# Performance work log

Measured on AMD Instinct MI355X. Metric: run time of the kernel, lower is better.

## Reference

```python
import jax, jax.numpy as jnp
import numpy as np

N, E, B = 50000, 400000, 128
F_IN, EDIM, EMB, H = 64, 8, 64, 4
HC = EMB * H  # 256
L = 3          # gnn_layers
DN = 256       # dense_neurons
NEG_SLOPE = 0.2
EPS = 1e-5


def setup_inputs():
    key = jax.random.key(0)
    ks = jax.random.split(key, 32)
    s = 0.05
    d = {}
    d["x"] = jax.random.normal(ks[0], (N, F_IN), jnp.float32)
    d["edge_index"] = jax.random.randint(ks[1], (2, E), 0, N, jnp.int32)
    d["edge_attr"] = jax.random.normal(ks[2], (E, EDIM), jnp.float32)
    d["mol_formal_charge"] = jax.random.normal(ks[3], (B,), jnp.float32)
    d["mol_nrot"] = jax.random.normal(ks[4], (B,), jnp.float32)
    d["batch_index"] = jnp.sort(jax.random.randint(ks[5], (N,), 0, B, jnp.int32))
    # GATv2 params, stacked over L layers (in_dim == EMB == F_IN for all layers)
    d["gat_Wl"] = jax.random.normal(ks[6], (L, F_IN, HC), jnp.float32) * s
    d["gat_Wr"] = jax.random.normal(ks[7], (L, F_IN, HC), jnp.float32) * s
    d["gat_We"] = jax.random.normal(ks[8], (L, EDIM, HC), jnp.float32) * s
    d["gat_att"] = jax.random.normal(ks[9], (L, H, EMB), jnp.float32) * s
    d["gat_b"] = jnp.zeros((L, HC), jnp.float32)
    d["tr_W"] = jax.random.normal(ks[10], (L, HC, EMB), jnp.float32) * s
    d["tr_b"] = jnp.zeros((L, EMB), jnp.float32)
    d["bn_g"] = jnp.ones((L, EMB), jnp.float32)
    d["bn_b"] = jnp.zeros((L, EMB), jnp.float32)
    d["gate_W"] = jax.random.normal(ks[11], (EMB, 1), jnp.float32) * s
    d["gate_b"] = jnp.zeros((1,), jnp.float32)
    d["lin1_W"] = jax.random.normal(ks[12], (EMB + 2, DN), jnp.float32) * s
    d["lin1_b"] = jnp.zeros((DN,), jnp.float32)
    d["fc1_W"] = jax.random.normal(ks[13], (DN, DN // 2), jnp.float32) * s
    d["fc1_b"] = jnp.zeros((DN // 2,), jnp.float32)
    d["fc2_W"] = jax.random.normal(ks[14], (DN // 2, DN // 4), jnp.float32) * s
    d["fc2_b"] = jnp.zeros((DN // 4,), jnp.float32)
    d["out_W"] = jax.random.normal(ks[15], (DN // 4, 1), jnp.float32) * s
    d["out_b"] = jnp.zeros((1,), jnp.float32)
    return d


def _seg_softmax(logits, seg, num):
    # numerically stable per-segment softmax over leading axis
    mx = jax.ops.segment_max(logits, seg, num_segments=num)
    ex = jnp.exp(logits - mx[seg])
    den = jax.ops.segment_sum(ex, seg, num_segments=num)
    return ex / den[seg]


def reference(x, edge_index, edge_attr, mol_formal_charge, mol_nrot, batch_index,
              gat_Wl, gat_Wr, gat_We, gat_att, gat_b, tr_W, tr_b, bn_g, bn_b,
              gate_W, gate_b, lin1_W, lin1_b, fc1_W, fc1_b, fc2_W, fc2_b,
              out_W, out_b):
    src, dst = edge_index[0], edge_index[1]  # messages flow src -> dst
    h = x
    for l in range(L):
        xl = (h @ gat_Wl[l]).reshape(N, H, EMB)
        xr = (h @ gat_Wr[l]).reshape(N, H, EMB)
        ea = (edge_attr @ gat_We[l]).reshape(E, H, EMB)
        xls = xl[src]                                   # [E,H,C]
        m = jax.nn.leaky_relu(xls + xr[dst] + ea, NEG_SLOPE)
        logit = jnp.einsum('ehc,hc->eh', m, gat_att[l])  # [E,H]
        alpha = _seg_softmax(logit, dst, N)              # [E,H]
        agg = jax.ops.segment_sum(alpha[:, :, None] * xls, dst, num_segments=N)
        h = agg.reshape(N, HC) + gat_b[l]
        h = jax.nn.relu(h @ tr_W[l] + tr_b[l])
        # BatchNorm1d (training-mode batch stats, biased var)
        mu = h.mean(0)
        var = h.var(0)
        h = (h - mu) / jnp.sqrt(var + EPS) * bn_g[l] + bn_b[l]
    # AttentionalAggregation pooling
    gate = h @ gate_W + gate_b                           # [N,1]
    w = _seg_softmax(gate, batch_index, B)
    pooled = jax.ops.segment_sum(w * h, batch_index, num_segments=B)  # [B,EMB]
    z = jnp.concatenate([pooled, mol_formal_charge[:, None], mol_nrot[:, None]], axis=1)
    z = jax.nn.relu(z @ lin1_W + lin1_b)
    z = jax.nn.relu(z @ fc1_W + fc1_b)
    z = jax.nn.relu(z @ fc2_W + fc2_b)
    return z @ out_W + out_b                             # [B,1]
```

## Files before the change

### kernel.cpp

```cpp
#include <hip/hip_runtime.h>

#define NN 50000
#define NE 400000
#define NB 128
#define NINF (-__builtin_inff())

__global__ __launch_bounds__(256) void k_hist(const int* __restrict__ dstv, int* __restrict__ deg) {
    int e = blockIdx.x * 256 + threadIdx.x;
    if (e < NE) atomicAdd(&deg[dstv[e]], 1);
}

__global__ __launch_bounds__(1024) void k_scan(const int* __restrict__ deg, int* __restrict__ rowptr) {
    __shared__ int wsum[16];
    __shared__ int total_s;
    const int tid = threadIdx.x, lane = tid & 63, w = tid >> 6;
    if (tid == 0) rowptr[0] = 0;
    int carry = 0;
    for (int base = 0; base < NN; base += 1024) {
        int i = base + tid;
        int v = (i < NN) ? deg[i] : 0;
        int incl = v;
        #pragma unroll
        for (int off = 1; off < 64; off <<= 1) {
            int t = __shfl_up(incl, off);
            if (lane >= off) incl += t;
        }
        if (lane == 63) wsum[w] = incl;
        __syncthreads();
        if (tid < 16) {
            int s = wsum[tid];
            int si = s;
            #pragma unroll
            for (int off = 1; off < 16; off <<= 1) {
                int t = __shfl_up(si, off, 16);
                if (tid >= off) si += t;
            }
            wsum[tid] = si - s;
            if (tid == 15) total_s = si;
        }
        __syncthreads();
        if (i < NN) rowptr[i + 1] = carry + wsum[w] + incl;
        carry += total_s;
        __syncthreads();
    }
}

__global__ __launch_bounds__(256) void k_scatter(const int* __restrict__ dstv, const int* __restrict__ rowptr,
                                                 int* __restrict__ cnt, int* __restrict__ eid) {
    int e = blockIdx.x * 256 + threadIdx.x;
    if (e < NE) {
        int d = dstv[e];
        int pos = rowptr[d] + atomicAdd(&cnt[d], 1);
        eid[pos] = e;
    }
}

__global__ __launch_bounds__(256) void k_permute(const int* __restrict__ eid, const int* __restrict__ srcv,
                                                 const float* __restrict__ eattr, int* __restrict__ src_perm,
                                                 float4* __restrict__ ea_perm) {
    int p = blockIdx.x * 256 + threadIdx.x;
    if (p < NE) {
        int e = eid[p];
        src_perm[p] = srcv[e];
        ea_perm[p * 2] = ((const float4*)eattr)[e * 2];
        ea_perm[p * 2 + 1] = ((const float4*)eattr)[e * 2 + 1];
    }
}

__global__ __launch_bounds__(256) void k_gemm64(const float* __restrict__ A, const float* __restrict__ Wl,
                                                const float* __restrict__ Wr, float* __restrict__ Cl,
                                                float* __restrict__ Cr, const float* __restrict__ bnp) {
    __shared__ float Ws[64 * 128];
    const int mat = blockIdx.y >> 1, ch = blockIdx.y & 1;
    const float* W = mat ? Wr : Wl;
    float* C = mat ? Cr : Cl;
    for (int i = threadIdx.x; i < 2048; i += 256) {
        const int k = i >> 5, c4 = i & 31;
        float4 v = ((const float4*)W)[k * 64 + ch * 32 + c4];
        if (bnp) {
            const float s = bnp[128 + k];
            v.x *= s; v.y *= s; v.z *= s; v.w *= s;
        }
        ((float4*)Ws)[i] = v;
    }
    __syncthreads();
    const int cg = threadIdx.x & 31;
    const int rq = threadIdx.x >> 5;
    const int r0 = blockIdx.x * 64 + rq * 8;

    float acc[8][4];
    if (bnp) {
        const float* shW = bnp + 256 + mat * 256 + ch * 128 + cg * 4;
        #pragma unroll
        for (int rr = 0; rr < 8; ++rr) {
            acc[rr][0] = shW[0]; acc[rr][1] = shW[1]; acc[rr][2] = shW[2]; acc[rr][3] = shW[3];
        }
    } else {
        #pragma unroll
        for (int rr = 0; rr < 8; ++rr)
            acc[rr][0] = acc[rr][1] = acc[rr][2] = acc[rr][3] = 0.f;
    }

    int rowc[8];
    #pragma unroll
    for (int rr = 0; rr < 8; ++rr) {
        int r = r0 + rr;
        rowc[rr] = (r < NN) ? r : (NN - 1);
    }

    for (int kq = 0; kq < 16; ++kq) {
        float4 av[8];
        #pragma unroll
        for (int rr = 0; rr < 8; ++rr)
            av[rr] = ((const float4*)A)[rowc[rr] * 16 + kq];
        #pragma unroll
        for (int kk = 0; kk < 4; ++kk) {
            const float4 w = *(const float4*)(Ws + ((kq * 4 + kk) << 7) + (cg << 2));
            #pragma unroll
            for (int rr = 0; rr < 8; ++rr) {
                const float a = reinterpret_cast<const float*>(&av[rr])[kk];
                acc[rr][0] = fmaf(a, w.x, acc[rr][0]);
                acc[rr][1] = fmaf(a, w.y, acc[rr][1]);
                acc[rr][2] = fmaf(a, w.z, acc[rr][2]);
                acc[rr][3] = fmaf(a, w.w, acc[rr][3]);
            }
        }
    }
    #pragma unroll
    for (int rr = 0; rr < 8; ++rr) {
        const int r = r0 + rr;
        if (r < NN)
            *(float4*)(C + (size_t)r * 256 + ch * 128 + cg * 4) =
                make_float4(acc[rr][0], acc[rr][1], acc[rr][2], acc[rr][3]);
    }
}

template <bool PERM>
__global__ __launch_bounds__(256, 4) void k_agg(const float* __restrict__ xl, float* __restrict__ xragg,
                                                const float* __restrict__ att, const float* __restrict__ gatb,
                                                const int* __restrict__ rowptr, const int* __restrict__ eid,
                                                const int* __restrict__ srcv, const float* __restrict__ eattr,
                                                const int* __restrict__ src_perm, const float4* __restrict__ ea_perm,
                                                const float* __restrict__ We) {
    const int lane = threadIdx.x & 63;
    const float4 we0 = ((const float4*)(We + 0 * 256))[lane];
    const float4 we1 = ((const float4*)(We + 1 * 256))[lane];
    const float4 we2 = ((const float4*)(We + 2 * 256))[lane];
    const float4 we3 = ((const float4*)(We + 3 * 256))[lane];
    const float4 we4 = ((const float4*)(We + 4 * 256))[lane];
    const float4 we5 = ((const float4*)(We + 5 * 256))[lane];
    const float4 we6 = ((const float4*)(We + 6 * 256))[lane];
    const float4 we7 = ((const float4*)(We + 7 * 256))[lane];
    const float4 attf = ((const float4*)att)[lane];
    const float4 gbf = ((const float4*)gatb)[lane];
    const int nw = gridDim.x * (blockDim.x >> 6);
    int wid = blockIdx.x * (blockDim.x >> 6) + (threadIdx.x >> 6);

    for (int n = wid; n < NN; n += nw) {
        const int e0 = rowptr[n], e1 = rowptr[n + 1];
        const float4 xr = ((const float4*)(xragg + (size_t)n * 256))[lane];
        float mrun = NINF, den = 0.f;
        float a0 = 0.f, a1 = 0.f, a2 = 0.f, a3 = 0.f;
        if (e1 > e0) {
            int s1 = 0, id1 = 0, id2 = 0;
            float4 xls_c, ea0_c, ea1_c;
            if (PERM) {
                const int s0 = src_perm[e0];
                s1 = (e0 + 1 < e1) ? src_perm[e0 + 1] : 0;
                xls_c = ((const float4*)(xl + (size_t)s0 * 256))[lane];
                ea0_c = ea_perm[(size_t)e0 * 2];
                ea1_c = ea_perm[(size_t)e0 * 2 + 1];
            } else {
                const int id0 = eid[e0];
                id1 = (e0 + 1 < e1) ? eid[e0 + 1] : 0;
                id2 = (e0 + 2 < e1) ? eid[e0 + 2] : 0;
                const int s0 = srcv[id0];
                s1 = (e0 + 1 < e1) ? srcv[id1] : 0;
                xls_c = ((const float4*)(xl + (size_t)s0 * 256))[lane];
                ea0_c = ((const float4*)(eattr + (size_t)id0 * 8))[0];
                ea1_c = ((const float4*)(eattr + (size_t)id0 * 8))[1];
            }
            for (int ei = e0; ei < e1; ++ei) {
                const bool h1 = (ei + 1 < e1), h2 = (ei + 2 < e1);
                float4 xls_n = xls_c, ea0_n = ea0_c, ea1_n = ea1_c;
                int s2 = 0, id3 = 0;
                if (h1) {
                    xls_n = ((const float4*)(xl + (size_t)s1 * 256))[lane];
                    if (PERM) {
                        ea0_n = ea_perm[(size_t)(ei + 1) * 2];
                        ea1_n = ea_perm[(size_t)(ei + 1) * 2 + 1];
                    } else {
                        ea0_n = ((const float4*)(eattr + (size_t)id1 * 8))[0];
                        ea1_n = ((const float4*)(eattr + (size_t)id1 * 8))[1];
                    }
                }
                if (h2) s2 = PERM ? src_perm[ei + 2] : srcv[id2];
                if (!PERM && (ei + 3 < e1)) id3 = eid[ei + 3];
                float ec0 = ea0_c.x * we0.x, ec1 = ea0_c.x * we0.y, ec2 = ea0_c.x * we0.z, ec3 = ea0_c.x * we0.w;
                ec0 = fmaf(ea0_c.y, we1.x, ec0); ec1 = fmaf(ea0_c.y, we1.y, ec1); ec2 = fmaf(ea0_c.y, we1.z, ec2); ec3 = fmaf(ea0_c.y, we1.w, ec3);
                ec0 = fmaf(ea0_c.z, we2.x, ec0); ec1 = fmaf(ea0_c.z, we2.y, ec1); ec2 = fmaf(ea0_c.z, we2.z, ec2); ec3 = fmaf(ea0_c.z, we2.w, ec3);
                ec0 = fmaf(ea0_c.w, we3.x, ec0); ec1 = fmaf(ea0_c.w, we3.y, ec1); ec2 = fmaf(ea0_c.w, we3.z, ec2); ec3 = fmaf(ea0_c.w, we3.w, ec3);
                ec0 = fmaf(ea1_c.x, we4.x, ec0); ec1 = fmaf(ea1_c.x, we4.y, ec1); ec2 = fmaf(ea1_c.x, we4.z, ec2); ec3 = fmaf(ea1_c.x, we4.w, ec3);
                ec0 = fmaf(ea1_c.y, we5.x, ec0); ec1 = fmaf(ea1_c.y, we5.y, ec1); ec2 = fmaf(ea1_c.y, we5.z, ec2); ec3 = fmaf(ea1_c.y, we5.w, ec3);
                ec0 = fmaf(ea1_c.z, we6.x, ec0); ec1 = fmaf(ea1_c.z, we6.y, ec1); ec2 = fmaf(ea1_c.z, we6.z, ec2); ec3 = fmaf(ea1_c.z, we6.w, ec3);
                ec0 = fmaf(ea1_c.w, we7.x, ec0); ec1 = fmaf(ea1_c.w, we7.y, ec1); ec2 = fmaf(ea1_c.w, we7.z, ec2); ec3 = fmaf(ea1_c.w, we7.w, ec3);
                float v0 = xls_c.x + xr.x + ec0;
                float v1 = xls_c.y + xr.y + ec1;
                float v2 = xls_c.z + xr.z + ec2;
                float v3 = xls_c.w + xr.w + ec3;
                v0 = fmaxf(v0, 0.2f * v0);
                v1 = fmaxf(v1, 0.2f * v1);
                v2 = fmaxf(v2, 0.2f * v2);
                v3 = fmaxf(v3, 0.2f * v3);
                float part = v0 * attf.x;
                part = fmaf(v1, attf.y, part);
                part = fmaf(v2, attf.z, part);
                part = fmaf(v3, attf.w, part);
                part += __shfl_xor(part, 1);
                part += __shfl_xor(part, 2);
                part += __shfl_xor(part, 4);
                part += __shfl_xor(part, 8);
                const float mn = fmaxf(mrun, part);
                const float scl = __expf(mrun - mn);
                const float p = __expf(part - mn);
                den = fmaf(den, scl, p);
                a0 = fmaf(a0, scl, p * xls_c.x);
                a1 = fmaf(a1, scl, p * xls_c.y);
                a2 = fmaf(a2, scl, p * xls_c.z);
                a3 = fmaf(a3, scl, p * xls_c.w);
                mrun = mn;
                xls_c = xls_n; ea0_c = ea0_n; ea1_c = ea1_n;
                s1 = s2; id1 = id2; id2 = id3;
            }
        }
        const float inv = (e1 > e0) ? (1.0f / den) : 0.f;
        float4 o;
        o.x = fmaf(a0, inv, gbf.x);
        o.y = fmaf(a1, inv, gbf.y);
        o.z = fmaf(a2, inv, gbf.z);
        o.w = fmaf(a3, inv, gbf.w);
        ((float4*)(xragg + (size_t)n * 256))[lane] = o;
    }
}

__global__ __launch_bounds__(256) void k_tr(const float* __restrict__ A, const float* __restrict__ W,
                                            const float* __restrict__ bias, float* __restrict__ Hout,
                                            float* __restrict__ stats) {
    __shared__ float Ws[64 * 64];
    __shared__ float red[128];
    const int cg = threadIdx.x & 15;
    const int rq = threadIdx.x >> 4;
    const int r0 = blockIdx.x * 128 + rq * 8;

    float acc[8][4];
    {
        const float b0 = bias[cg * 4], b1 = bias[cg * 4 + 1], b2 = bias[cg * 4 + 2], b3 = bias[cg * 4 + 3];
        #pragma unroll
        for (int rr = 0; rr < 8; ++rr) { acc[rr][0] = b0; acc[rr][1] = b1; acc[rr][2] = b2; acc[rr][3] = b3; }
    }
    int rowc[8];
    #pragma unroll
    for (int rr = 0; rr < 8; ++rr) {
        int r = r0 + rr;
        rowc[rr] = (r < NN) ? r : (NN - 1);
    }

    for (int kc = 0; kc < 4; ++kc) {
        __syncthreads();
        for (int i = threadIdx.x; i < 1024; i += 256)
            ((float4*)Ws)[i] = ((const float4*)(W + kc * 4096))[i];
        __syncthreads();
        for (int kq = 0; kq < 16; ++kq) {
            float4 av[8];
            #pragma unroll
            for (int rr = 0; rr < 8; ++rr)
                av[rr] = ((const float4*)A)[(size_t)rowc[rr] * 64 + kc * 16 + kq];
            #pragma unroll
            for (int kk = 0; kk < 4; ++kk) {
                const float4 w = *(const float4*)(Ws + ((kq * 4 + kk) << 6) + (cg << 2));
                #pragma unroll
                for (int rr = 0; rr < 8; ++rr) {
                    const float a = reinterpret_cast<const float*>(&av[rr])[kk];
                    acc[rr][0] = fmaf(a, w.x, acc[rr][0]);
                    acc[rr][1] = fmaf(a, w.y, acc[rr][1]);
                    acc[rr][2] = fmaf(a, w.z, acc[rr][2]);
                    acc[rr][3] = fmaf(a, w.w, acc[rr][3]);
                }
            }
        }
    }
    float lsum[4] = {0.f, 0.f, 0.f, 0.f}, lsq[4] = {0.f, 0.f, 0.f, 0.f};
    #pragma unroll
    for (int rr = 0; rr < 8; ++rr) {
        const int r = r0 + rr;
        if (r < NN) {
            float v0 = fmaxf(acc[rr][0], 0.f), v1 = fmaxf(acc[rr][1], 0.f);
            float v2 = fmaxf(acc[rr][2], 0.f), v3 = fmaxf(acc[rr][3], 0.f);
            lsum[0] += v0; lsum[1] += v1; lsum[2] += v2; lsum[3] += v3;
            lsq[0] = fmaf(v0, v0, lsq[0]); lsq[1] = fmaf(v1, v1, lsq[1]);
            lsq[2] = fmaf(v2, v2, lsq[2]); lsq[3] = fmaf(v3, v3, lsq[3]);
            *(float4*)(Hout + (size_t)r * 64 + cg * 4) = make_float4(v0, v1, v2, v3);
        }
    }
    __syncthreads();
    if (threadIdx.x < 128) red[threadIdx.x] = 0.f;
    __syncthreads();
    #pragma unroll
    for (int j = 0; j < 4; ++j) {
        atomicAdd(&red[cg * 4 + j], lsum[j]);
        atomicAdd(&red[64 + cg * 4 + j], lsq[j]);
    }
    __syncthreads();
    if (threadIdx.x < 64) {
        atomicAdd(&stats[threadIdx.x], red[threadIdx.x]);
        atomicAdd(&stats[64 + threadIdx.x], red[64 + threadIdx.x]);
    }
}

__global__ __launch_bounds__(256) void k_bn_finalize(float* __restrict__ st, const float* __restrict__ g,
                                                     const float* __restrict__ b, const float* __restrict__ Wln,
                                                     const float* __restrict__ Wrn) {
    __shared__ float sh_s[64];
    const int tid = threadIdx.x;
    if (tid < 64) {
        const float mu = st[tid] * (1.0f / (float)NN);
        const float var = st[64 + tid] * (1.0f / (float)NN) - mu * mu;
        const float rstd = rsqrtf(var + 1e-5f);
        const float sc = g[tid] * rstd;
        const float sh = fmaf(-mu, sc, b[tid]);
        st[128 + tid] = sc;
        st[192 + tid] = sh;
        sh_s[tid] = sh;
    }
    __syncthreads();
    if (Wln) {
        float al = 0.f, ar = 0.f;
        for (int k = 0; k < 64; ++k) {
            al = fmaf(sh_s[k], Wln[k * 256 + tid], al);
            ar = fmaf(sh_s[k], Wrn[k * 256 + tid], ar);
        }
        st[256 + tid] = al;
        st[512 + tid] = ar;
    }
}

__global__ __launch_bounds__(256) void k_pool(const float* __restrict__ h, const float* __restrict__ gw,
                                              const int* __restrict__ bidx, const float* __restrict__ st,
                                              float* __restrict__ pooled) {
    __shared__ float gate_s[1024];
    __shared__ float red[4];
    __shared__ float pp[4][64];
    const int b = blockIdx.x, tid = threadIdx.x, lane = tid & 63, w = tid >> 6;
    int lo = 0, hi = NN;
    while (lo < hi) { int mid = (lo + hi) >> 1; if (bidx[mid] < b) lo = mid + 1; else hi = mid; }
    const int s0 = lo;
    lo = 0; hi = NN;
    while (lo < hi) { int mid = (lo + hi) >> 1; if (bidx[mid] < b + 1) lo = mid + 1; else hi = mid; }
    const int s1 = lo;
    const int seg = s1 - s0;
    if (seg == 0) {
        if (tid < 64) pooled[b * 64 + tid] = st[192 + tid];
        return;
    }
    const float gwv = gw[lane] * st[128 + lane];
    for (int i = s0 + w; i < s1; i += 4) {
        float p = h[(size_t)i * 64 + lane] * gwv;
        #pragma unroll
        for (int off = 32; off; off >>= 1) p += __shfl_xor(p, off);
        if (lane == 0) gate_s[i - s0] = p;
    }
    __syncthreads();
    float v = NINF;
    for (int i = tid; i < seg; i += 256) v = fmaxf(v, gate_s[i]);
    #pragma unroll
    for (int off = 32; off; off >>= 1) v = fmaxf(v, __shfl_xor(v, off));
    if (lane == 0) red[w] = v;
    __syncthreads();
    const float mx = fmaxf(fmaxf(red[0], red[1]), fmaxf(red[2], red[3]));
    __syncthreads();
    float d = 0.f;
    for (int i = tid; i < seg; i += 256) {
        const float ex = __expf(gate_s[i] - mx);
        gate_s[i] = ex;
        d += ex;
    }
    #pragma unroll
    for (int off = 32; off; off >>= 1) d += __shfl_xor(d, off);
    if (lane == 0) red[w] = d;
    __syncthreads();
    const float den = red[0] + red[1] + red[2] + red[3];
    const int c = tid & 63, ro = tid >> 6;
    float acc = 0.f;
    for (int i = s0 + ro; i < s1; i += 4) acc = fmaf(gate_s[i - s0], h[(size_t)i * 64 + c], acc);
    pp[ro][c] = acc;
    __syncthreads();
    if (ro == 0) {
        const float raw = (pp[0][c] + pp[1][c] + pp[2][c] + pp[3][c]) / den;
        pooled[b * 64 + c] = fmaf(raw, st[128 + c], st[192 + c]);
    }
}

__global__ __launch_bounds__(256) void k_head(const float* __restrict__ pooled, const float* __restrict__ fc,
                                              const float* __restrict__ nrot, const float* __restrict__ W1,
                                              const float* __restrict__ b1, const float* __restrict__ W2,
                                              const float* __restrict__ b2, const float* __restrict__ W3,
                                              const float* __restrict__ b3, const float* __restrict__ W4,
                                              const float* __restrict__ b4, float* __restrict__ out) {
    __shared__ float z[66], a1[256], a2[128], a3[64];
    const int b = blockIdx.x, tid = threadIdx.x;
    if (tid < 64) z[tid] = pooled[b * 64 + tid];
    if (tid == 64) z[64] = fc[b];
    if (tid == 65) z[65] = nrot[b];
    __syncthreads();
    float s = b1[tid];
    for (int k = 0; k < 66; ++k) s = fmaf(z[k], W1[k * 256 + tid], s);
    a1[tid] = fmaxf(s, 0.f);
    __syncthreads();
    if (tid < 128) {
        float s2 = b2[tid];
        for (int k = 0; k < 256; ++k) s2 = fmaf(a1[k], W2[k * 128 + tid], s2);
        a2[tid] = fmaxf(s2, 0.f);
    }
    __syncthreads();
    if (tid < 64) {
        float s3 = b3[tid];
        for (int k = 0; k < 128; ++k) s3 = fmaf(a2[k], W3[k * 64 + tid], s3);
        a3[tid] = fmaxf(s3, 0.f);
    }
    __syncthreads();
    if (tid < 64) {
        float p = a3[tid] * W4[tid];
        #pragma unroll
        for (int off = 32; off; off >>= 1) p += __shfl_xor(p, off);
        if (tid == 0) out[b] = p + b4[0];
    }
}

extern "C" void kernel_launch(void* const* d_in, const int* in_sizes, int n_in,
                              void* d_out, int out_size, void* d_ws, size_t ws_size,
                              hipStream_t stream) {
    const float* x     = (const float*)d_in[0];
    const int*   ei    = (const int*)d_in[1];
    const float* eattr = (const float*)d_in[2];
    const float* fcv   = (const float*)d_in[3];
    const float* nrot  = (const float*)d_in[4];
    const int*   bidx  = (const int*)d_in[5];
    const float* Wl    = (const float*)d_in[6];
    const float* Wr    = (const float*)d_in[7];
    const float* We    = (const float*)d_in[8];
    const float* att   = (const float*)d_in[9];
    const float* gatb  = (const float*)d_in[10];
    const float* trW   = (const float*)d_in[11];
    const float* trb   = (const float*)d_in[12];
    const float* bng   = (const float*)d_in[13];
    const float* bnb   = (const float*)d_in[14];
    const float* gateW = (const float*)d_in[15];
    const float* W1    = (const float*)d_in[17];
    const float* b1    = (const float*)d_in[18];
    const float* W2    = (const float*)d_in[19];
    const float* b2    = (const float*)d_in[20];
    const float* W3    = (const float*)d_in[21];
    const float* b3    = (const float*)d_in[22];
    const float* W4    = (const float*)d_in[23];
    const float* b4    = (const float*)d_in[24];
    float* out = (float*)d_out;

    const int* srcv = ei;
    const int* dstv = ei + NE;

    char* w = (char*)d_ws;
    float*  xl       = (float*)(w);
    float*  xragg    = (float*)(w + 51200000);
    float*  hbuf     = (float*)(w + 102400000);
    int*    deg      = (int*)  (w + 102400000);
    int*    cnt      = (int*)  (w + 102600000);
    int*    eid      = (int*)  (w + 115200000);
    int*    rowptr   = (int*)  (w + 116800000);
    float*  stats    = (float*)(w + 117000064);
    float*  pooled   = (float*)(w + 117009280);
    int*    src_perm = (int*)  (w + 117042048);
    float4* ea_perm  = (float4*)(w + 118642048);
    const bool use_perm = (ws_size >= (size_t)131442048);

    hipMemsetAsync(deg, 0, 400000, stream);
    hipMemsetAsync(stats, 0, 9216, stream);
    k_hist<<<(NE + 255) / 256, 256, 0, stream>>>(dstv, deg);
    k_scan<<<1, 1024, 0, stream>>>(deg, rowptr);
    k_scatter<<<(NE + 255) / 256, 256, 0, stream>>>(dstv, rowptr, cnt, eid);
    if (use_perm)
        k_permute<<<(NE + 255) / 256, 256, 0, stream>>>(eid, srcv, eattr, src_perm, ea_perm);

    const float* hin = x;
    for (int l = 0; l < 3; ++l) {
        const float* bnp = (l == 0) ? nullptr : (stats + (l - 1) * 768);
        dim3 gg((NN + 63) / 64, 4);
        k_gemm64<<<gg, 256, 0, stream>>>(hin, Wl + l * 16384, Wr + l * 16384, xl, xragg, bnp);
        if (use_perm)
            k_agg<true><<<2048, 256, 0, stream>>>(xl, xragg, att + l * 256, gatb + l * 256, rowptr,
                                                  eid, srcv, eattr, src_perm, ea_perm, We + l * 2048);
        else
            k_agg<false><<<2048, 256, 0, stream>>>(xl, xragg, att + l * 256, gatb + l * 256, rowptr,
                                                   eid, srcv, eattr, src_perm, ea_perm, We + l * 2048);
        k_tr<<<(NN + 127) / 128, 256, 0, stream>>>(xragg, trW + l * 16384, trb + l * 64, hbuf, stats + l * 768);
        k_bn_finalize<<<1, 256, 0, stream>>>(stats + l * 768, bng + l * 64, bnb + l * 64,
                                             (l < 2) ? (Wl + (l + 1) * 16384) : nullptr,
                                             (l < 2) ? (Wr + (l + 1) * 16384) : nullptr);
        hin = hbuf;
    }
    k_pool<<<NB, 256, 0, stream>>>(hbuf, gateW, bidx, stats + 2 * 768, pooled);
    k_head<<<NB, 256, 0, stream>>>(pooled, fcv, nrot, W1, b1, W2, b2, W3, b3, W4, b4, out);
}
```

Baseline: 789.9 us.

## Stage GEMM inputs in LDS and split edge aggregation into two online-softmax streams

The node-feature GEMM and the transform GEMM now stage their A tiles into shared memory instead of each thread reading strided rows from global memory. The transform kernel also moves to 64-row blocks, doubling its grid. The edge aggregation loop is restructured to keep two independent online-softmax accumulators, fed by a deeper software-pipelined prefetch that loads two edges ahead, and the two are merged at the end. This adds ILP and memory-level parallelism to the latency-bound gather, at the cost of more registers and possible occupancy loss.

```diff
diff --git a/kernel.cpp b/kernel.cpp
--- a/kernel.cpp
+++ b/kernel.cpp
@@ -70,11 +70,15 @@
 __global__ __launch_bounds__(256) void k_gemm64(const float* __restrict__ A, const float* __restrict__ Wl,
                                                 const float* __restrict__ Wr, float* __restrict__ Cl,
                                                 float* __restrict__ Cr, const float* __restrict__ bnp) {
+    __shared__ float As[64 * 64];
     __shared__ float Ws[64 * 128];
+    const int tid = threadIdx.x;
     const int mat = blockIdx.y >> 1, ch = blockIdx.y & 1;
     const float* W = mat ? Wr : Wl;
     float* C = mat ? Cr : Cl;
-    for (int i = threadIdx.x; i < 2048; i += 256) {
+    const int r0b = blockIdx.x * 64;
+
+    for (int i = tid; i < 2048; i += 256) {
         const int k = i >> 5, c4 = i & 31;
         float4 v = ((const float4*)W)[k * 64 + ch * 32 + c4];
         if (bnp) {
@@ -83,11 +87,15 @@
         }
         ((float4*)Ws)[i] = v;
     }
-    __syncthreads();
-    const int cg = threadIdx.x & 31;
-    const int rq = threadIdx.x >> 5;
-    const int r0 = blockIdx.x * 64 + rq * 8;
-
+    for (int i = tid; i < 1024; i += 256) {
+        const int r = i >> 4, c4 = i & 15;
+        const int rg = (r0b + r < NN) ? (r0b + r) : (NN - 1);
+        ((float4*)As)[i] = ((const float4*)A)[rg * 16 + c4];
+    }
+    __syncthreads();
+
+    const int cg = tid & 31;
+    const int rq = tid >> 5;
     float acc[8][4];
     if (bnp) {
         const float* shW = bnp + 256 + mat * 256 + ch * 128 + cg * 4;
@@ -101,18 +109,11 @@
             acc[rr][0] = acc[rr][1] = acc[rr][2] = acc[rr][3] = 0.f;
     }
 
-    int rowc[8];
-    #pragma unroll
-    for (int rr = 0; rr < 8; ++rr) {
-        int r = r0 + rr;
-        rowc[rr] = (r < NN) ? r : (NN - 1);
-    }
-
     for (int kq = 0; kq < 16; ++kq) {
         float4 av[8];
         #pragma unroll
         for (int rr = 0; rr < 8; ++rr)
-            av[rr] = ((const float4*)A)[rowc[rr] * 16 + kq];
+            av[rr] = ((const float4*)As)[(rq * 8 + rr) * 16 + kq];
         #pragma unroll
         for (int kk = 0; kk < 4; ++kk) {
             const float4 w = *(const float4*)(Ws + ((kq * 4 + kk) << 7) + (cg << 2));
@@ -128,7 +129,7 @@
     }
     #pragma unroll
     for (int rr = 0; rr < 8; ++rr) {
-        const int r = r0 + rr;
+        const int r = r0b + rq * 8 + rr;
         if (r < NN)
             *(float4*)(C + (size_t)r * 256 + ch * 128 + cg * 4) =
                 make_float4(acc[rr][0], acc[rr][1], acc[rr][2], acc[rr][3]);
@@ -156,130 +157,145 @@
     const int nw = gridDim.x * (blockDim.x >> 6);
     int wid = blockIdx.x * (blockDim.x >> 6) + (threadIdx.x >> 6);
 
+#define LOADE(X, idx)                                                          \
+    {                                                                          \
+        int s_;                                                                \
+        const float4* eap_;                                                    \
+        if (PERM) {                                                            \
+            s_ = src_perm[idx];                                                \
+            eap_ = ea_perm + (size_t)(idx) * 2;                                \
+        } else {                                                               \
+            const int e_ = eid[idx];                                           \
+            s_ = srcv[e_];                                                     \
+            eap_ = (const float4*)(eattr + (size_t)e_ * 8);                    \
+        }                                                                      \
+        X##x = ((const float4*)(xl + (size_t)s_ * 256))[lane];                 \
+        X##a = eap_[0];                                                        \
+        X##b = eap_[1];                                                        \
+    }
+
+#define PROC(X, M, D, C0, C1, C2, C3)                                          \
+    {                                                                          \
+        float v0 = fmaf(X##a.x, we0.x, xr.x), v1 = fmaf(X##a.x, we0.y, xr.y);  \
+        float v2 = fmaf(X##a.x, we0.z, xr.z), v3 = fmaf(X##a.x, we0.w, xr.w);  \
+        v0 = fmaf(X##a.y, we1.x, v0); v1 = fmaf(X##a.y, we1.y, v1);            \
+        v2 = fmaf(X##a.y, we1.z, v2); v3 = fmaf(X##a.y, we1.w, v3);            \
+        v0 = fmaf(X##a.z, we2.x, v0); v1 = fmaf(X##a.z, we2.y, v1);            \
+        v2 = fmaf(X##a.z, we2.z, v2); v3 = fmaf(X##a.z, we2.w, v3);            \
+        v0 = fmaf(X##a.w, we3.x, v0); v1 = fmaf(X##a.w, we3.y, v1);            \
+        v2 = fmaf(X##a.w, we3.z, v2); v3 = fmaf(X##a.w, we3.w, v3);            \
+        v0 = fmaf(X##b.x, we4.x, v0); v1 = fmaf(X##b.x, we4.y, v1);            \
+        v2 = fmaf(X##b.x, we4.z, v2); v3 = fmaf(X##b.x, we4.w, v3);            \
+        v0 = fmaf(X##b.y, we5.x, v0); v1 = fmaf(X##b.y, we5.y, v1);            \
+        v2 = fmaf(X##b.y, we5.z, v2); v3 = fmaf(X##b.y, we5.w, v3);            \
+        v0 = fmaf(X##b.z, we6.x, v0); v1 = fmaf(X##b.z, we6.y, v1);            \
+        v2 = fmaf(X##b.z, we6.z, v2); v3 = fmaf(X##b.z, we6.w, v3);            \
+        v0 = fmaf(X##b.w, we7.x, v0); v1 = fmaf(X##b.w, we7.y, v1);            \
+        v2 = fmaf(X##b.w, we7.z, v2); v3 = fmaf(X##b.w, we7.w, v3);            \
+        v0 += X##x.x; v1 += X##x.y; v2 += X##x.z; v3 += X##x.w;                \
+        v0 = fmaxf(v0, 0.2f * v0); v1 = fmaxf(v1, 0.2f * v1);                  \
+        v2 = fmaxf(v2, 0.2f * v2); v3 = fmaxf(v3, 0.2f * v3);                  \
+        float part = v0 * attf.x;                                              \
+        part = fmaf(v1, attf.y, part);                                         \
+        part = fmaf(v2, attf.z, part);                                         \
+        part = fmaf(v3, attf.w, part);                                         \
+        part += __shfl_xor(part, 1);                                           \
+        part += __shfl_xor(part, 2);                                           \
+        part += __shfl_xor(part, 4);                                           \
+        part += __shfl_xor(part, 8);                                           \
+        const float mn = fmaxf(M, part);                                       \
+        const float scl = __expf(M - mn);                                      \
+        const float p = __expf(part - mn);                                     \
+        D = fmaf(D, scl, p);                                                   \
+        C0 = fmaf(C0, scl, p * X##x.x);                                        \
+        C1 = fmaf(C1, scl, p * X##x.y);                                        \
+        C2 = fmaf(C2, scl, p * X##x.z);                                        \
+        C3 = fmaf(C3, scl, p * X##x.w);                                        \
+        M = mn;                                                                \
+    }
+
     for (int n = wid; n < NN; n += nw) {
         const int e0 = rowptr[n], e1 = rowptr[n + 1];
         const float4 xr = ((const float4*)(xragg + (size_t)n * 256))[lane];
-        float mrun = NINF, den = 0.f;
-        float a0 = 0.f, a1 = 0.f, a2 = 0.f, a3 = 0.f;
+        float mA = NINF, dA = 0.f, cA0 = 0.f, cA1 = 0.f, cA2 = 0.f, cA3 = 0.f;
+        float mB = NINF, dB = 0.f, cB0 = 0.f, cB1 = 0.f, cB2 = 0.f, cB3 = 0.f;
+        float4 Ax, Aa, Ab, Bx, Ba, Bb;
+        if (e0 < e1) LOADE(A, e0);
+        if (e0 + 1 < e1) LOADE(B, e0 + 1);
+        int i = e0;
+        for (; i + 5 < e1; i += 4) {
+            float4 Cx, Ca, Cb, Dx, Da, Db;
+            LOADE(C, i + 2);
+            LOADE(D, i + 3);
+            PROC(A, mA, dA, cA0, cA1, cA2, cA3);
+            PROC(B, mB, dB, cB0, cB1, cB2, cB3);
+            LOADE(A, i + 4);
+            LOADE(B, i + 5);
+            PROC(C, mA, dA, cA0, cA1, cA2, cA3);
+            PROC(D, mB, dB, cB0, cB1, cB2, cB3);
+        }
+        if (i < e1) PROC(A, mA, dA, cA0, cA1, cA2, cA3);
+        if (i + 1 < e1) PROC(B, mB, dB, cB0, cB1, cB2, cB3);
+        for (int j = i + 2; j < e1; ++j) {
+            LOADE(A, j);
+            PROC(A, mA, dA, cA0, cA1, cA2, cA3);
+        }
+        float4 o;
         if (e1 > e0) {
-            int s1 = 0, id1 = 0, id2 = 0;
-            float4 xls_c, ea0_c, ea1_c;
-            if (PERM) {
-                const int s0 = src_perm[e0];
-                s1 = (e0 + 1 < e1) ? src_perm[e0 + 1] : 0;
-                xls_c = ((const float4*)(xl + (size_t)s0 * 256))[lane];
-                ea0_c = ea_perm[(size_t)e0 * 2];
-                ea1_c = ea_perm[(size_t)e0 * 2 + 1];
-            } else {
-                const int id0 = eid[e0];
-                id1 = (e0 + 1 < e1) ? eid[e0 + 1] : 0;
-                id2 = (e0 + 2 < e1) ? eid[e0 + 2] : 0;
-                const int s0 = srcv[id0];
-                s1 = (e0 + 1 < e1) ? srcv[id1] : 0;
-                xls_c = ((const float4*)(xl + (size_t)s0 * 256))[lane];
-                ea0_c = ((const float4*)(eattr + (size_t)id0 * 8))[0];
-                ea1_c = ((const float4*)(eattr + (size_t)id0 * 8))[1];
-            }
-            for (int ei = e0; ei < e1; ++ei) {
-                const bool h1 = (ei + 1 < e1), h2 = (ei + 2 < e1);
-                float4 xls_n = xls_c, ea0_n = ea0_c, ea1_n = ea1_c;
-                int s2 = 0, id3 = 0;
-                if (h1) {
-                    xls_n = ((const float4*)(xl + (size_t)s1 * 256))[lane];
-                    if (PERM) {
-                        ea0_n = ea_perm[(size_t)(ei + 1) * 2];
-                        ea1_n = ea_perm[(size_t)(ei + 1) * 2 + 1];
-                    } else {
-                        ea0_n = ((const float4*)(eattr + (size_t)id1 * 8))[0];
-                        ea1_n = ((const float4*)(eattr + (size_t)id1 * 8))[1];
-                    }
-                }
-                if (h2) s2 = PERM ? src_perm[ei + 2] : srcv[id2];
-                if (!PERM && (ei + 3 < e1)) id3 = eid[ei + 3];
-                float ec0 = ea0_c.x * we0.x, ec1 = ea0_c.x * we0.y, ec2 = ea0_c.x * we0.z, ec3 = ea0_c.x * we0.w;
-                ec0 = fmaf(ea0_c.y, we1.x, ec0); ec1 = fmaf(ea0_c.y, we1.y, ec1); ec2 = fmaf(ea0_c.y, we1.z, ec2); ec3 = fmaf(ea0_c.y, we1.w, ec3);
-                ec0 = fmaf(ea0_c.z, we2.x, ec0); ec1 = fmaf(ea0_c.z, we2.y, ec1); ec2 = fmaf(ea0_c.z, we2.z, ec2); ec3 = fmaf(ea0_c.z, we2.w, ec3);
-                ec0 = fmaf(ea0_c.w, we3.x, ec0); ec1 = fmaf(ea0_c.w, we3.y, ec1); ec2 = fmaf(ea0_c.w, we3.z, ec2); ec3 = fmaf(ea0_c.w, we3.w, ec3);
-                ec0 = fmaf(ea1_c.x, we4.x, ec0); ec1 = fmaf(ea1_c.x, we4.y, ec1); ec2 = fmaf(ea1_c.x, we4.z, ec2); ec3 = fmaf(ea1_c.x, we4.w, ec3);
-                ec0 = fmaf(ea1_c.y, we5.x, ec0); ec1 = fmaf(ea1_c.y, we5.y, ec1); ec2 = fmaf(ea1_c.y, we5.z, ec2); ec3 = fmaf(ea1_c.y, we5.w, ec3);
-                ec0 = fmaf(ea1_c.z, we6.x, ec0); ec1 = fmaf(ea1_c.z, we6.y, ec1); ec2 = fmaf(ea1_c.z, we6.z, ec2); ec3 = fmaf(ea1_c.z, we6.w, ec3);
-                ec0 = fmaf(ea1_c.w, we7.x, ec0); ec1 = fmaf(ea1_c.w, we7.y, ec1); ec2 = fmaf(ea1_c.w, we7.z, ec2); ec3 = fmaf(ea1_c.w, we7.w, ec3);
-                float v0 = xls_c.x + xr.x + ec0;
-                float v1 = xls_c.y + xr.y + ec1;
-                float v2 = xls_c.z + xr.z + ec2;
-                float v3 = xls_c.w + xr.w + ec3;
-                v0 = fmaxf(v0, 0.2f * v0);
-                v1 = fmaxf(v1, 0.2f * v1);
-                v2 = fmaxf(v2, 0.2f * v2);
-                v3 = fmaxf(v3, 0.2f * v3);
-                float part = v0 * attf.x;
-                part = fmaf(v1, attf.y, part);
-                part = fmaf(v2, attf.z, part);
-                part = fmaf(v3, attf.w, part);
-                part += __shfl_xor(part, 1);
-                part += __shfl_xor(part, 2);
-                part += __shfl_xor(part, 4);
-                part += __shfl_xor(part, 8);
-                const float mn = fmaxf(mrun, part);
-                const float scl = __expf(mrun - mn);
-                const float p = __expf(part - mn);
-                den = fmaf(den, scl, p);
-                a0 = fmaf(a0, scl, p * xls_c.x);
-                a1 = fmaf(a1, scl, p * xls_c.y);
-                a2 = fmaf(a2, scl, p * xls_c.z);
-                a3 = fmaf(a3, scl, p * xls_c.w);
-                mrun = mn;
-                xls_c = xls_n; ea0_c = ea0_n; ea1_c = ea1_n;
-                s1 = s2; id1 = id2; id2 = id3;
-            }
-        }
-        const float inv = (e1 > e0) ? (1.0f / den) : 0.f;
-        float4 o;
-        o.x = fmaf(a0, inv, gbf.x);
-        o.y = fmaf(a1, inv, gbf.y);
-        o.z = fmaf(a2, inv, gbf.z);
-        o.w = fmaf(a3, inv, gbf.w);
+            const float m = fmaxf(mA, mB);
+            const float wA = __expf(mA - m), wB = __expf(mB - m);
+            const float inv = 1.0f / fmaf(wA, dA, wB * dB);
+            o.x = fmaf((wA * cA0 + wB * cB0), inv, gbf.x);
+            o.y = fmaf((wA * cA1 + wB * cB1), inv, gbf.y);
+            o.z = fmaf((wA * cA2 + wB * cB2), inv, gbf.z);
+            o.w = fmaf((wA * cA3 + wB * cB3), inv, gbf.w);
+        } else {
+            o = gbf;
+        }
         ((float4*)(xragg + (size_t)n * 256))[lane] = o;
     }
+#undef LOADE
+#undef PROC
 }
 
 __global__ __launch_bounds__(256) void k_tr(const float* __restrict__ A, const float* __restrict__ W,
                                             const float* __restrict__ bias, float* __restrict__ Hout,
                                             float* __restrict__ stats) {
+    __shared__ float As[64 * 68];
     __shared__ float Ws[64 * 64];
     __shared__ float red[128];
-    const int cg = threadIdx.x & 15;
-    const int rq = threadIdx.x >> 4;
-    const int r0 = blockIdx.x * 128 + rq * 8;
-
-    float acc[8][4];
+    const int tid = threadIdx.x;
+    const int cg = tid & 15;
+    const int rq = tid >> 4;
+    const int r0b = blockIdx.x * 64;
+
+    float acc[4][4];
     {
         const float b0 = bias[cg * 4], b1 = bias[cg * 4 + 1], b2 = bias[cg * 4 + 2], b3 = bias[cg * 4 + 3];
         #pragma unroll
-        for (int rr = 0; rr < 8; ++rr) { acc[rr][0] = b0; acc[rr][1] = b1; acc[rr][2] = b2; acc[rr][3] = b3; }
-    }
-    int rowc[8];
-    #pragma unroll
-    for (int rr = 0; rr < 8; ++rr) {
-        int r = r0 + rr;
-        rowc[rr] = (r < NN) ? r : (NN - 1);
+        for (int rr = 0; rr < 4; ++rr) { acc[rr][0] = b0; acc[rr][1] = b1; acc[rr][2] = b2; acc[rr][3] = b3; }
     }
 
     for (int kc = 0; kc < 4; ++kc) {
-        __syncthreads();
-        for (int i = threadIdx.x; i < 1024; i += 256)
+        if (kc) __syncthreads();
+        for (int i = tid; i < 1024; i += 256)
             ((float4*)Ws)[i] = ((const float4*)(W + kc * 4096))[i];
+        for (int i = tid; i < 1024; i += 256) {
+            const int r = i >> 4, c4 = i & 15;
+            const int rg = (r0b + r < NN) ? (r0b + r) : (NN - 1);
+            *(float4*)(As + r * 68 + c4 * 4) = ((const float4*)A)[(size_t)rg * 64 + kc * 16 + c4];
+        }
         __syncthreads();
         for (int kq = 0; kq < 16; ++kq) {
-            float4 av[8];
+            float4 av[4];
             #pragma unroll
-            for (int rr = 0; rr < 8; ++rr)
-                av[rr] = ((const float4*)A)[(size_t)rowc[rr] * 64 + kc * 16 + kq];
+            for (int rr = 0; rr < 4; ++rr)
+                av[rr] = *(const float4*)(As + (rq * 4 + rr) * 68 + kq * 4);
             #pragma unroll
             for (int kk = 0; kk < 4; ++kk) {
                 const float4 w = *(const float4*)(Ws + ((kq * 4 + kk) << 6) + (cg << 2));
                 #pragma unroll
-                for (int rr = 0; rr < 8; ++rr) {
+                for (int rr = 0; rr < 4; ++rr) {
                     const float a = reinterpret_cast<const float*>(&av[rr])[kk];
                     acc[rr][0] = fmaf(a, w.x, acc[rr][0]);
                     acc[rr][1] = fmaf(a, w.y, acc[rr][1]);
@@ -291,8 +307,8 @@
     }
     float lsum[4] = {0.f, 0.f, 0.f, 0.f}, lsq[4] = {0.f, 0.f, 0.f, 0.f};
     #pragma unroll
-    for (int rr = 0; rr < 8; ++rr) {
-        const int r = r0 + rr;
+    for (int rr = 0; rr < 4; ++rr) {
+        const int r = r0b + rq * 4 + rr;
         if (r < NN) {
             float v0 = fmaxf(acc[rr][0], 0.f), v1 = fmaxf(acc[rr][1], 0.f);
             float v2 = fmaxf(acc[rr][2], 0.f), v3 = fmaxf(acc[rr][3], 0.f);
@@ -303,7 +319,7 @@
         }
     }
     __syncthreads();
-    if (threadIdx.x < 128) red[threadIdx.x] = 0.f;
+    if (tid < 128) red[tid] = 0.f;
     __syncthreads();
     #pragma unroll
     for (int j = 0; j < 4; ++j) {
@@ -311,9 +327,9 @@
         atomicAdd(&red[64 + cg * 4 + j], lsq[j]);
     }
     __syncthreads();
-    if (threadIdx.x < 64) {
-        atomicAdd(&stats[threadIdx.x], red[threadIdx.x]);
-        atomicAdd(&stats[64 + threadIdx.x], red[64 + threadIdx.x]);
+    if (tid < 64) {
+        atomicAdd(&stats[tid], red[tid]);
+        atomicAdd(&stats[64 + tid], red[64 + tid]);
     }
 }
 
@@ -501,7 +517,7 @@
         else
             k_agg<false><<<2048, 256, 0, stream>>>(xl, xragg, att + l * 256, gatb + l * 256, rowptr,
                                                    eid, srcv, eattr, src_perm, ea_perm, We + l * 2048);
-        k_tr<<<(NN + 127) / 128, 256, 0, stream>>>(xragg, trW + l * 16384, trb + l * 64, hbuf, stats + l * 768);
+        k_tr<<<(NN + 63) / 64, 256, 0, stream>>>(xragg, trW + l * 16384, trb + l * 64, hbuf, stats + l * 768);
         k_bn_finalize<<<1, 256, 0, stream>>>(stats + l * 768, bng + l * 64, bnb + l * 64,
                                              (l < 2) ? (Wl + (l + 1) * 16384) : nullptr,
                                              (l < 2) ? (Wr + (l + 1) * 16384) : nullptr);
```

After: 792.3 us. No clear change (+0.3%).
